# Kernel optimization log

Hardware: AMD Instinct MI355X
Metric: run time of the kernel (lower is better)

## Reference

```python
import jax, jax.numpy as jnp
import numpy as np

B, S, HID = 2, 2048, 3584
NH, NKV, HD = 16, 8, 256
WINDOW = 1024
SOFTCAP = 50.0


def setup_inputs() -> dict:
    key = jax.random.key(0)
    ks = jax.random.split(key, 8)
    hidden_states = jax.random.normal(ks[0], (B, S, HID), dtype=jnp.float32)
    attention_mask = jnp.ones((B, S), dtype=bool)
    position_ids = jnp.tile(jnp.arange(S, dtype=jnp.int32), (B, 1))
    # rotary tables indexed by position, last dim = head_dim
    inv_freq = 1.0 / (10000.0 ** (jnp.arange(0, HD, 2, dtype=jnp.float32) / HD))
    t = jnp.arange(S, dtype=jnp.float32)
    freqs = jnp.outer(t, inv_freq)  # [S, HD/2]
    emb = jnp.concatenate([freqs, freqs], axis=-1)  # [S, HD]
    sin, cos = jnp.sin(emb), jnp.cos(emb)
    causal_mask = jnp.tril(jnp.ones((1, 1, S, S), dtype=bool))
    sc = 0.02
    Wq = jax.random.normal(ks[1], (HID, NH * HD), dtype=jnp.float32) * sc
    Wk = jax.random.normal(ks[2], (HID, NKV * HD), dtype=jnp.float32) * sc
    Wv = jax.random.normal(ks[3], (HID, NKV * HD), dtype=jnp.float32) * sc
    Wo = jax.random.normal(ks[4], (NH * HD, HID), dtype=jnp.float32) * sc
    return {"hidden_states": hidden_states, "attention_mask": attention_mask,
            "position_ids": position_ids, "sin": sin, "cos": cos,
            "causal_mask": causal_mask, "Wq": Wq, "Wk": Wk, "Wv": Wv, "Wo": Wo}


def _rotate_half(x):
    x1, x2 = x[..., : x.shape[-1] // 2], x[..., x.shape[-1] // 2 :]
    return jnp.concatenate((-x2, x1), axis=-1)


def reference(hidden_states, attention_mask, position_ids, sin, cos, causal_mask, Wq, Wk, Wv, Wo):
    b, s, _ = hidden_states.shape
    q = (hidden_states @ Wq).reshape(b, s, NH, HD)
    k = (hidden_states @ Wk).reshape(b, s, NKV, HD)
    v = (hidden_states @ Wv).reshape(b, s, NKV, HD)

    # RoPE, applied in [b, h, s, d] layout as in the original
    s_ = sin[position_ids][:, None, :, :]  # [b,1,s,d]
    c_ = cos[position_ids][:, None, :, :]
    qh = q.transpose(0, 2, 1, 3)
    kh = k.transpose(0, 2, 1, 3)
    qh = qh * c_ + _rotate_half(qh) * s_
    kh = kh * c_ + _rotate_half(kh) * s_
    q = qh.transpose(0, 2, 1, 3)  # [b,s,nh,d]
    k = kh.transpose(0, 2, 1, 3)  # [b,s,nkv,d]

    # GQA: repeat kv heads to match query heads
    groups = NH // NKV
    k = jnp.repeat(k, groups, axis=2)  # [b,s,nh,d]
    v = jnp.repeat(v, groups, axis=2)

    # combine causal + padding masks, then sliding-window (even layer)
    mask = causal_mask[:, :, :s, :s] & attention_mask[:, None, None, :]  # [b,1,s,s]
    mask = jnp.broadcast_to(mask, (b, 1, s, s))
    far_past = jnp.tril(jnp.ones((s, s), dtype=bool), k=-WINDOW)[None, None]
    mask = mask & ~far_past

    neg = jnp.finfo(jnp.float32).min
    bias = jnp.where(mask, 0.0, neg).astype(jnp.float32)

    scale = HD ** -0.5
    logits = jnp.einsum("bqhd,bkhd->bhqk", q, k) * scale
    # Gemma2 logit softcapping
    logits = SOFTCAP * jnp.tanh(logits / SOFTCAP)
    logits = logits + bias
    probs = jax.nn.softmax(logits, axis=-1)
    out = jnp.einsum("bhqk,bkhd->bqhd", probs, v)
    out = out.reshape(b, s, NH * HD)
    return out @ Wo
```

## Files before the change

kernel.cpp:

```cpp
#include <hip/hip_runtime.h>
#include <hip/hip_bf16.h>

typedef __bf16 bf16x8_t __attribute__((ext_vector_type(8)));
typedef __bf16 bf16x4_t __attribute__((ext_vector_type(4)));
typedef short s16x4_t  __attribute__((ext_vector_type(4)));
typedef float f32x4_t  __attribute__((ext_vector_type(4)));

#define NB 2
#define NS 2048
#define NHID 3584
#define NHEADS 16
#define NKVH 8
#define DH 256
#define WIN 1024

__device__ __forceinline__ float bf2f(ushort u) {
  union { unsigned v; float f; } x; x.v = ((unsigned)u) << 16; return x.f;
}
__device__ __forceinline__ ushort f2bf(float f) {
  unsigned x = __builtin_bit_cast(unsigned, f);
  unsigned r = (x + 0x7fffu + ((x >> 16) & 1u)) >> 16;
  return (ushort)r;
}

__device__ __forceinline__ void gload16(const void* g, void* l) {
  __builtin_amdgcn_global_load_lds((const __attribute__((address_space(1))) void*)g,
                                   (__attribute__((address_space(3))) void*)l, 16, 0, 0);
}

__device__ __forceinline__ f32x4_t mfma_pv(s16x4_t a, s16x4_t b, f32x4_t c) {
#if __has_builtin(__builtin_amdgcn_mfma_f32_16x16x16_bf16)
  return __builtin_amdgcn_mfma_f32_16x16x16_bf16(
      __builtin_bit_cast(bf16x4_t, a), __builtin_bit_cast(bf16x4_t, b), c, 0, 0, 0);
#else
  return __builtin_amdgcn_mfma_f32_16x16x16bf16_1k(a, b, c, 0, 0, 0);
#endif
}

__device__ __forceinline__ float pexp(float s) {
  float e = __expf(fminf(s * 0.0025f, 80.f));
  float th = __fdividef(e - 1.f, e + 1.f);
  return __expf(50.f * th);
}

__global__ __launch_bounds__(256) void f32_to_bf16_kernel(const float* __restrict__ in,
                                                          ushort* __restrict__ out, int n4) {
  int i = (int)blockIdx.x * 256 + (int)threadIdx.x;
  if (i < n4) {
    float4 v = ((const float4*)in)[i];
    ushort4 o;
    o.x = f2bf(v.x); o.y = f2bf(v.y); o.z = f2bf(v.z); o.w = f2bf(v.w);
    ((ushort4*)out)[i] = o;
  }
}

__global__ __launch_bounds__(256) void transpose_f32_bf16(const float* __restrict__ in,
                                                          ushort* __restrict__ out,
                                                          int R, int Cc) {
  __shared__ ushort tile[64][72];
  const int t = threadIdx.x;
  const int ct = Cc >> 6;
  const int by = blockIdx.x / ct;
  const int bx = blockIdx.x % ct;
  const int r0 = by << 6, c0 = bx << 6;
#pragma unroll
  for (int i = 0; i < 16; ++i) {
    int idx = i * 256 + t;
    int r = idx >> 6, c = idx & 63;
    tile[r][c] = f2bf(in[(size_t)(r0 + r) * Cc + c0 + c]);
  }
  __syncthreads();
#pragma unroll
  for (int i = 0; i < 16; ++i) {
    int idx = i * 256 + t;
    int rr = idx >> 6, cc = idx & 63;
    out[(size_t)(c0 + rr) * R + r0 + cc] = tile[cc][rr];
  }
}

#define GSYNC1 do { __builtin_amdgcn_s_barrier(); \
    asm volatile("s_waitcnt lgkmcnt(0)" ::: "memory"); \
    __builtin_amdgcn_sched_barrier(0); } while (0)
#define GSYNC2(st) do { \
    if (st) asm volatile("s_waitcnt vmcnt(2)" ::: "memory"); \
    else    asm volatile("s_waitcnt vmcnt(0)" ::: "memory"); \
    __builtin_amdgcn_sched_barrier(0); \
    __builtin_amdgcn_s_barrier(); } while (0)

template <int EPI>
__global__ __launch_bounds__(512, 2) void gemm256(const ushort* __restrict__ A,
                                                  const ushort* __restrict__ Bt,
                                                  void* __restrict__ Cout,
                                                  const float* __restrict__ sinT,
                                                  const float* __restrict__ cosT,
                                                  int M, int N, int K) {
  __shared__ alignas(16) char lds[131072];
  const int t = threadIdx.x;
  const int lane = t & 63;
  const int wid = t >> 6;
  const int wm = wid >> 2;
  const int wn = wid & 3;
  const int g = lane >> 4;
  const int lr = lane & 15;
  const int lrow8 = lane >> 3;
  const int lp = (lane & 7) ^ lrow8;

  const int nbn = N >> 8;
  const int nwg = (int)gridDim.x;
  const int bid = (int)blockIdx.x;
  const int swz = (bid & 7) * (nwg >> 3) + (bid >> 3);
  const int bm = swz / nbn, bn = swz % nbn;
  const int m0 = bm << 8, n0 = bn << 8;

  f32x4_t acc[8][4] = {};
  const int T = K >> 6;

  auto stageA = [&](int q, int koff, int bufn) {
    int row = (q << 6) + (wid << 3) + lrow8;
    gload16(A + (size_t)(m0 + row) * K + koff + (lp << 3),
            lds + bufn * 32768 + (q << 13) + (wid << 10));
  };
  auto stageB = [&](int q, int koff, int bufn) {
    int row = (q << 6) + (wid << 3) + lrow8;
    gload16(Bt + (size_t)(n0 + row) * K + koff + (lp << 3),
            lds + 65536 + bufn * 32768 + (q << 13) + (wid << 10));
  };

#pragma unroll
  for (int q = 0; q < 4; ++q) { stageA(q, 0, 0); stageB(q, 0, 0); }
  asm volatile("s_waitcnt vmcnt(0)" ::: "memory");
  __builtin_amdgcn_s_barrier();

  for (int tt = 0; tt < T; ++tt) {
    const int bc = tt & 1;
    const int bnx = bc ^ 1;
    const bool st = (tt + 1 < T);
    const int kn = (tt + 1) << 6;
    const char* cA = lds + bc * 32768;
    const char* cB = lds + 65536 + bc * 32768;
    bf16x8_t af[4], bfv[4];

    auto ldA = [&](int i, int mh, int ks) {
      int row = (wm << 7) + (mh << 6) + (i << 4) + lr;
      af[i] = *(const bf16x8_t*)(cA + (row << 7) + (((ks << 6) + (g << 4)) ^ ((row & 7) << 4)));
    };
    auto ldB = [&](int j, int ks) {
      int row = (wn << 6) + (j << 4) + lr;
      bfv[j] = *(const bf16x8_t*)(cB + (row << 7) + (((ks << 6) + (g << 4)) ^ ((row & 7) << 4)));
    };

#pragma unroll
    for (int i = 0; i < 4; ++i) ldA(i, 0, 0);
#pragma unroll
    for (int j = 0; j < 4; ++j) ldB(j, 0);
    if (st) { stageA(0, kn, bnx); stageA(2, kn, bnx); }
    GSYNC1;
    __builtin_amdgcn_s_setprio(1);
#pragma unroll
    for (int i = 0; i < 4; ++i)
#pragma unroll
      for (int j = 0; j < 4; ++j)
        acc[i][j] = __builtin_amdgcn_mfma_f32_16x16x32_bf16(af[i], bfv[j], acc[i][j], 0, 0, 0);
    __builtin_amdgcn_s_setprio(0);
    GSYNC2(st);

#pragma unroll
    for (int i = 0; i < 4; ++i) ldA(i, 1, 0);
    if (st) { stageB(0, kn, bnx); stageB(1, kn, bnx); }
    GSYNC1;
    __builtin_amdgcn_s_setprio(1);
#pragma unroll
    for (int i = 0; i < 4; ++i)
#pragma unroll
      for (int j = 0; j < 4; ++j)
        acc[4 + i][j] = __builtin_amdgcn_mfma_f32_16x16x32_bf16(af[i], bfv[j], acc[4 + i][j], 0, 0, 0);
    __builtin_amdgcn_s_setprio(0);
    GSYNC2(st);

#pragma unroll
    for (int i = 0; i < 4; ++i) ldA(i, 0, 1);
#pragma unroll
    for (int j = 0; j < 4; ++j) ldB(j, 1);
    if (st) { stageB(2, kn, bnx); stageB(3, kn, bnx); }
    GSYNC1;
    __builtin_amdgcn_s_setprio(1);
#pragma unroll
    for (int i = 0; i < 4; ++i)
#pragma unroll
      for (int j = 0; j < 4; ++j)
        acc[i][j] = __builtin_amdgcn_mfma_f32_16x16x32_bf16(af[i], bfv[j], acc[i][j], 0, 0, 0);
    __builtin_amdgcn_s_setprio(0);
    GSYNC2(st);

#pragma unroll
    for (int i = 0; i < 4; ++i) ldA(i, 1, 1);
    if (st) { stageA(1, kn, bnx); stageA(3, kn, bnx); }
    GSYNC1;
    __builtin_amdgcn_s_setprio(1);
#pragma unroll
    for (int i = 0; i < 4; ++i)
#pragma unroll
      for (int j = 0; j < 4; ++j)
        acc[4 + i][j] = __builtin_amdgcn_mfma_f32_16x16x32_bf16(af[i], bfv[j], acc[4 + i][j], 0, 0, 0);
    __builtin_amdgcn_s_setprio(0);
    GSYNC2(st);
  }

  __syncthreads();
  const bool trstage = (EPI == 5) && (n0 >= 2048);
  if (trstage) {
#pragma unroll
    for (int i = 0; i < 8; ++i)
#pragma unroll
      for (int j = 0; j < 4; ++j) {
        int col = (wn << 6) + (j << 4) + lr;
#pragma unroll
        for (int r = 0; r < 4; ++r) {
          int row = (wm << 7) + (i << 4) + (g << 2) + r;
          *(ushort*)(lds + (col << 9) + ((row << 1) ^ ((col & 7) << 4))) = f2bf(acc[i][j][r]);
        }
      }
  } else {
#pragma unroll
    for (int i = 0; i < 8; ++i)
#pragma unroll
      for (int j = 0; j < 4; ++j) {
        int col = (wn << 6) + (j << 4) + lr;
#pragma unroll
        for (int r = 0; r < 4; ++r) {
          int row = (wm << 7) + (i << 4) + (g << 2) + r;
          *(ushort*)(lds + (row << 9) + ((col << 1) ^ ((row & 7) << 4))) = f2bf(acc[i][j][r]);
        }
      }
  }
  __syncthreads();

  auto ropeStore = [&](ushort* C, int ldc) {
#pragma unroll
    for (int it = 0; it < 16; ++it) {
      int idx = it * 512 + t;
      int row = idx >> 5, ch = idx & 31;
      uint4 v = *(const uint4*)(lds + (row << 9) + ((ch << 4) ^ ((row & 7) << 4)));
      uint4 p = *(const uint4*)(lds + (row << 9) + (((ch ^ 16) << 4) ^ ((row & 7) << 4)));
      int pos = (m0 + row) & (NS - 1);
      int d0 = ch << 3;
      float4 c0 = *(const float4*)(cosT + (size_t)pos * 256 + d0);
      float4 c1 = *(const float4*)(cosT + (size_t)pos * 256 + d0 + 4);
      float4 s0 = *(const float4*)(sinT + (size_t)pos * 256 + d0);
      float4 s1 = *(const float4*)(sinT + (size_t)pos * 256 + d0 + 4);
      float cs[8] = {c0.x, c0.y, c0.z, c0.w, c1.x, c1.y, c1.z, c1.w};
      float ss[8] = {s0.x, s0.y, s0.z, s0.w, s1.x, s1.y, s1.z, s1.w};
      const float sgn = (ch < 16) ? -1.f : 1.f;
      const ushort* vv = (const ushort*)&v;
      const ushort* pp = (const ushort*)&p;
      ushort o[8];
#pragma unroll
      for (int e = 0; e < 8; ++e)
        o[e] = f2bf(bf2f(vv[e]) * cs[e] + sgn * bf2f(pp[e]) * ss[e]);
      *(uint4*)(C + (size_t)(m0 + row) * ldc + n0 % ((EPI == 5) ? 2048 : (1 << 30)) + (ch << 3)) = *(const uint4*)o;
    }
  };

  if (EPI == 1) {
    ushort* C = (ushort*)Cout;
#pragma unroll
    for (int it = 0; it < 16; ++it) {
      int idx = it * 512 + t;
      int row = idx >> 5, ch = idx & 31;
      uint4 v = *(const uint4*)(lds + (row << 9) + ((ch << 4) ^ ((row & 7) << 4)));
      uint4 p = *(const uint4*)(lds + (row << 9) + (((ch ^ 16) << 4) ^ ((row & 7) << 4)));
      int pos = (m0 + row) & (NS - 1);
      int d0 = ch << 3;
      float4 c0 = *(const float4*)(cosT + (size_t)pos * 256 + d0);
      float4 c1 = *(const float4*)(cosT + (size_t)pos * 256 + d0 + 4);
      float4 s0 = *(const float4*)(sinT + (size_t)pos * 256 + d0);
      float4 s1 = *(const float4*)(sinT + (size_t)pos * 256 + d0 + 4);
      float cs[8] = {c0.x, c0.y, c0.z, c0.w, c1.x, c1.y, c1.z, c1.w};
      float ss[8] = {s0.x, s0.y, s0.z, s0.w, s1.x, s1.y, s1.z, s1.w};
      const float sgn = (ch < 16) ? -1.f : 1.f;
      const ushort* vv = (const ushort*)&v;
      const ushort* pp = (const ushort*)&p;
      ushort o[8];
#pragma unroll
      for (int e = 0; e < 8; ++e)
        o[e] = f2bf(bf2f(vv[e]) * cs[e] + sgn * bf2f(pp[e]) * ss[e]);
      *(uint4*)(C + (size_t)(m0 + row) * N + n0 + (ch << 3)) = *(const uint4*)o;
    }
  } else if (EPI == 5) {
    ushort* C = (ushort*)Cout;
    if (n0 < 2048) {
#pragma unroll
      for (int it = 0; it < 16; ++it) {
        int idx = it * 512 + t;
        int row = idx >> 5, ch = idx & 31;
        uint4 v = *(const uint4*)(lds + (row << 9) + ((ch << 4) ^ ((row & 7) << 4)));
        uint4 p = *(const uint4*)(lds + (row << 9) + (((ch ^ 16) << 4) ^ ((row & 7) << 4)));
        int pos = (m0 + row) & (NS - 1);
        int d0 = ch << 3;
        float4 c0 = *(const float4*)(cosT + (size_t)pos * 256 + d0);
        float4 c1 = *(const float4*)(cosT + (size_t)pos * 256 + d0 + 4);
        float4 s0 = *(const float4*)(sinT + (size_t)pos * 256 + d0);
        float4 s1 = *(const float4*)(sinT + (size_t)pos * 256 + d0 + 4);
        float cs[8] = {c0.x, c0.y, c0.z, c0.w, c1.x, c1.y, c1.z, c1.w};
        float ss[8] = {s0.x, s0.y, s0.z, s0.w, s1.x, s1.y, s1.z, s1.w};
        const float sgn = (ch < 16) ? -1.f : 1.f;
        const ushort* vv = (const ushort*)&v;
        const ushort* pp = (const ushort*)&p;
        ushort o[8];
#pragma unroll
        for (int e = 0; e < 8; ++e)
          o[e] = f2bf(bf2f(vv[e]) * cs[e] + sgn * bf2f(pp[e]) * ss[e]);
        *(uint4*)(C + (size_t)(m0 + row) * 2048 + n0 + (ch << 3)) = *(const uint4*)o;
      }
    } else {
      ushort* vC = C + (size_t)4096 * 2048;
      const int plane = (m0 >> 11) * NKVH + ((n0 - 2048) >> 8);
      ushort* dst = vC + (size_t)plane * ((size_t)NS * DH) + (size_t)((m0 & (NS - 1)) >> 5) * 8192;
#pragma unroll
      for (int it = 0; it < 16; ++it) {
        int s = it * 512 + t;
        int lr2 = s & 7, kq = (s >> 3) & 7, dt_l = (s >> 6) & 15, sb_l = s >> 10;
        int d0 = (dt_l << 4) + (lr2 << 1);
        int r0 = (sb_l << 5) + (kq << 2);
        uint2 a = *(const uint2*)(lds + (d0 << 9) + ((r0 << 1) ^ ((d0 & 7) << 4)));
        uint2 b2 = *(const uint2*)(lds + ((d0 + 1) << 9) + ((r0 << 1) ^ (((d0 + 1) & 7) << 4)));
        uint4 v; v.x = a.x; v.y = a.y; v.z = b2.x; v.w = b2.y;
        *(uint4*)(dst + (size_t)s * 8) = v;
      }
    }
  } else {
    float* Cf = (float*)Cout;
#pragma unroll
    for (int it = 0; it < 32; ++it) {
      int idx = it * 512 + t;
      int row = idx >> 6, qd = idx & 63;
      ushort4 hv = *(const ushort4*)(lds + (row << 9) + ((qd << 3) ^ ((row & 7) << 4)));
      float4 fv;
      fv.x = bf2f(hv.x); fv.y = bf2f(hv.y); fv.z = bf2f(hv.z); fv.w = bf2f(hv.w);
      *(float4*)(Cf + (size_t)(m0 + row) * N + n0 + (qd << 2)) = fv;
    }
  }
}

__global__ __launch_bounds__(512) void attn_kernel(const ushort* __restrict__ q,
                                                   const ushort* __restrict__ k,
                                                   const ushort* __restrict__ vt,
                                                   ushort* __restrict__ ao) {
  __shared__ alignas(16) char lK[2][16384];
  __shared__ alignas(16) char lV[2][16384];
  const int bid = (int)blockIdx.x;
  const int qb = bid & 15;
  const int h = (bid >> 4) & 15;
  const int b = bid >> 8;
  const int kvh = h >> 1;
  const int qb0 = qb << 7;
  const int t = threadIdx.x;
  const int lane = t & 63;
  const int w = t >> 6;
  const int g = lane >> 4;
  const int lr = lane & 15;

  const int qrow = qb0 + (w << 4) + lr;
  bf16x8_t qf[8];
  const ushort* qbase = q + (size_t)(b * NS + qrow) * (NHEADS * DH) + h * DH;
#pragma unroll
  for (int ks = 0; ks < 8; ++ks)
    qf[ks] = *(const bf16x8_t*)(qbase + (ks << 5) + (g << 3));

  float l_r = 0.f;
  f32x4_t oacc[16] = {};

  const int qminw = qb0 + (w << 4);
  const int qmaxw = qminw + 15;
  int t_lo = qb0 - (WIN - 1);
  if (t_lo < 0) t_lo = 0;
  t_lo &= ~31;
  const int t_hi = qb0 + 127;
  const int nt = ((t_hi - t_lo) >> 5) + 1;

  const ushort* kgb = k + (size_t)(b * NS) * (NKVH * DH) + kvh * DH;
  const ushort* vgb = vt + (size_t)(b * NKVH + kvh) * ((size_t)NS * DH);

  auto stage = [&](int kt, int bi) {
    char* dk = lK[bi];
    char* dv = lV[bi];
    const int sb = kt >> 5;
#pragma unroll
    for (int j = 0; j < 2; ++j) {
      int i = (w << 1) + j;
      int row = (i << 1) + (lane >> 5);
      int ck = (lane & 31) ^ (row & 7);
      gload16(kgb + (size_t)(kt + row) * (NKVH * DH) + (ck << 3), dk + (i << 10));
      gload16(vgb + (size_t)sb * 8192 + (((i << 6) + lane) << 3), dv + (i << 10));
    }
  };

  int cur = 0;
  stage(t_lo, 0);
  __syncthreads();

  for (int i = 0; i < nt; ++i) {
    const int kt = t_lo + (i << 5);
    if (i + 1 < nt) stage(kt + 32, cur ^ 1);
    const char* lk = lK[cur];
    const char* lv = lV[cur];
#pragma unroll
    for (int sub = 0; sub < 2; ++sub) {
      const int key0 = kt + (sub << 4);
      if (key0 > qmaxw) continue;
      if (key0 + 15 < qminw - (WIN - 1)) continue;

      f32x4_t sacc = {};
      __builtin_amdgcn_s_setprio(1);
#pragma unroll
      for (int ks = 0; ks < 8; ++ks) {
        int row = (sub << 4) + lr;
        bf16x8_t kf = *(const bf16x8_t*)(lk + (((row << 9) + (ks << 6) + (g << 4)) ^ ((row & 7) << 4)));
        sacc = __builtin_amdgcn_mfma_f32_16x16x32_bf16(kf, qf[ks], sacc, 0, 0, 0);
      }
      __builtin_amdgcn_s_setprio(0);

      float pvv[4];
      const bool full = (key0 + 15 <= qminw) && (key0 >= qmaxw - (WIN - 1));
      if (full) {
#pragma unroll
        for (int r = 0; r < 4; ++r) { pvv[r] = pexp(sacc[r]); l_r += pvv[r]; }
      } else {
#pragma unroll
        for (int r = 0; r < 4; ++r) {
          int key = key0 + (g << 2) + r;
          bool ok = (key <= qrow) && (qrow - key < WIN);
          pvv[r] = ok ? pexp(sacc[r]) : 0.f;
          l_r += pvv[r];
        }
      }

      s16x4_t pa;
      pa[0] = (short)f2bf(pvv[0]);
      pa[1] = (short)f2bf(pvv[1]);
      pa[2] = (short)f2bf(pvv[2]);
      pa[3] = (short)f2bf(pvv[3]);

      const int kqoff = ((sub << 2) + g) << 7;
      __builtin_amdgcn_s_setprio(1);
#pragma unroll
      for (int dt = 0; dt < 16; ++dt) {
        s16x4_t vf = *(const s16x4_t*)(lv + (dt << 10) + kqoff + (lr << 3));
        oacc[dt] = mfma_pv(pa, vf, oacc[dt]);
      }
      __builtin_amdgcn_s_setprio(0);
    }
    __syncthreads();
    cur ^= 1;
  }

  l_r += __shfl_xor(l_r, 16);
  l_r += __shfl_xor(l_r, 32);
  float dn[4];
#pragma unroll
  for (int r = 0; r < 4; ++r)
    dn[r] = 1.0f / __shfl(l_r, (g << 2) + r);

  const int orow0 = b * NS + qb0 + (w << 4) + (g << 2);
#pragma unroll
  for (int dt = 0; dt < 16; ++dt) {
    int col = h * DH + (dt << 4) + lr;
#pragma unroll
    for (int r = 0; r < 4; ++r) {
      ao[(size_t)(orow0 + r) * (NHEADS * DH) + col] = f2bf(oacc[dt][r] * dn[r]);
    }
  }
}

extern "C" void kernel_launch(void* const* d_in, const int* in_sizes, int n_in,
                              void* d_out, int out_size, void* d_ws, size_t ws_size,
                              hipStream_t stream) {
  const float* hs   = (const float*)d_in[0];
  const float* sint = (const float*)d_in[3];
  const float* cost = (const float*)d_in[4];
  const float* Wq = (const float*)d_in[6];
  const float* Wk = (const float*)d_in[7];
  const float* Wv = (const float*)d_in[8];
  const float* Wo = (const float*)d_in[9];

  char* ws = (char*)d_ws;
  size_t off = 0;
  auto alloc = [&](size_t bytes) {
    char* p = ws + off;
    off += (bytes + 255) & ~(size_t)255;
    return p;
  };
  ushort* hsb   = (ushort*)alloc((size_t)4096 * 3584 * 2);
  ushort* wT    = (ushort*)alloc((size_t)4096 * 3584 * 2);
  ushort* qbuf  = (ushort*)alloc((size_t)4096 * 4096 * 2);
  ushort* kbuf  = (ushort*)alloc((size_t)4096 * 2048 * 2);
  ushort* vtbuf = (ushort*)alloc((size_t)4096 * 2048 * 2);
  ushort* aobuf = qbuf;
  if (off > ws_size) return;

  f32_to_bf16_kernel<<<(4096 * 3584 / 4) / 256, 256, 0, stream>>>(hs, hsb, 4096 * 3584 / 4);

  transpose_f32_bf16<<<(3584 / 64) * (2048 / 64), 256, 0, stream>>>(Wk, wT, 3584, 2048);
  transpose_f32_bf16<<<(3584 / 64) * (2048 / 64), 256, 0, stream>>>(Wv, wT + (size_t)2048 * 3584, 3584, 2048);
  gemm256<5><<<16 * 16, 512, 0, stream>>>(hsb, wT, kbuf, sint, cost, 4096, 4096, 3584);

  transpose_f32_bf16<<<(3584 / 64) * (4096 / 64), 256, 0, stream>>>(Wq, wT, 3584, 4096);
  gemm256<1><<<16 * 16, 512, 0, stream>>>(hsb, wT, qbuf, sint, cost, 4096, 4096, 3584);

  attn_kernel<<<NB * NHEADS * (NS / 128), 512, 0, stream>>>(qbuf, kbuf, vtbuf, aobuf);

  transpose_f32_bf16<<<(4096 / 64) * (3584 / 64), 256, 0, stream>>>(Wo, wT, 4096, 3584);
  gemm256<2><<<16 * 14, 512, 0, stream>>>(aobuf, wT, d_out, nullptr, nullptr, 4096, 3584, 4096);
}
```

Baseline: 587.3 us.

## Halve attention query tile to 64 rows and reorder blocks for load balance

The attention kernel now uses 64-row query tiles with 256 threads per block, doubling the grid to 1024 blocks. Block IDs are remapped so expensive late-sequence tiles are scheduled first, paired head blocks share a KV plane, and cheaper early tiles fill in later, aiming to balance the sliding-window workload across CUs and improve L2 reuse of K/V. Each block stages K/V with more loads per thread. Smaller tiles mean K/V is reloaded from memory more often per query row. An unused ropeStore lambda is also removed.

```diff
diff --git a/kernel.cpp b/kernel.cpp
--- a/kernel.cpp
+++ b/kernel.cpp
@@ -235,7 +235,8 @@
   }
   __syncthreads();
 
-  auto ropeStore = [&](ushort* C, int ldc) {
+  if (EPI == 1) {
+    ushort* C = (ushort*)Cout;
 #pragma unroll
     for (int it = 0; it < 16; ++it) {
       int idx = it * 512 + t;
@@ -257,33 +258,6 @@
 #pragma unroll
       for (int e = 0; e < 8; ++e)
         o[e] = f2bf(bf2f(vv[e]) * cs[e] + sgn * bf2f(pp[e]) * ss[e]);
-      *(uint4*)(C + (size_t)(m0 + row) * ldc + n0 % ((EPI == 5) ? 2048 : (1 << 30)) + (ch << 3)) = *(const uint4*)o;
-    }
-  };
-
-  if (EPI == 1) {
-    ushort* C = (ushort*)Cout;
-#pragma unroll
-    for (int it = 0; it < 16; ++it) {
-      int idx = it * 512 + t;
-      int row = idx >> 5, ch = idx & 31;
-      uint4 v = *(const uint4*)(lds + (row << 9) + ((ch << 4) ^ ((row & 7) << 4)));
-      uint4 p = *(const uint4*)(lds + (row << 9) + (((ch ^ 16) << 4) ^ ((row & 7) << 4)));
-      int pos = (m0 + row) & (NS - 1);
-      int d0 = ch << 3;
-      float4 c0 = *(const float4*)(cosT + (size_t)pos * 256 + d0);
-      float4 c1 = *(const float4*)(cosT + (size_t)pos * 256 + d0 + 4);
-      float4 s0 = *(const float4*)(sinT + (size_t)pos * 256 + d0);
-      float4 s1 = *(const float4*)(sinT + (size_t)pos * 256 + d0 + 4);
-      float cs[8] = {c0.x, c0.y, c0.z, c0.w, c1.x, c1.y, c1.z, c1.w};
-      float ss[8] = {s0.x, s0.y, s0.z, s0.w, s1.x, s1.y, s1.z, s1.w};
-      const float sgn = (ch < 16) ? -1.f : 1.f;
-      const ushort* vv = (const ushort*)&v;
-      const ushort* pp = (const ushort*)&p;
-      ushort o[8];
-#pragma unroll
-      for (int e = 0; e < 8; ++e)
-        o[e] = f2bf(bf2f(vv[e]) * cs[e] + sgn * bf2f(pp[e]) * ss[e]);
       *(uint4*)(C + (size_t)(m0 + row) * N + n0 + (ch << 3)) = *(const uint4*)o;
     }
   } else if (EPI == 5) {
@@ -342,18 +316,28 @@
   }
 }
 
-__global__ __launch_bounds__(512) void attn_kernel(const ushort* __restrict__ q,
+__global__ __launch_bounds__(256) void attn_kernel(const ushort* __restrict__ q,
                                                    const ushort* __restrict__ k,
                                                    const ushort* __restrict__ vt,
                                                    ushort* __restrict__ ao) {
   __shared__ alignas(16) char lK[2][16384];
   __shared__ alignas(16) char lV[2][16384];
   const int bid = (int)blockIdx.x;
-  const int qb = bid & 15;
-  const int h = (bid >> 4) & 15;
-  const int b = bid >> 8;
-  const int kvh = h >> 1;
-  const int qb0 = qb << 7;
+  const int x = bid & 7;
+  const int s_ = bid >> 3;
+  const int rnd = s_ >> 5;
+  const int c = s_ & 31;
+  const int a = c >> 1;
+  const int hl = c & 1;
+  const int plane = (x << 1) | (rnd & 1);
+  int qb;
+  if (rnd < 2) qb = 16 + a;
+  else if (rnd == 2) qb = a;
+  else qb = 15 - a;
+  const int b = plane >> 3;
+  const int kvh = plane & 7;
+  const int h = (kvh << 1) | hl;
+  const int qb0 = qb << 6;
   const int t = threadIdx.x;
   const int lane = t & 63;
   const int w = t >> 6;
@@ -375,7 +359,7 @@
   int t_lo = qb0 - (WIN - 1);
   if (t_lo < 0) t_lo = 0;
   t_lo &= ~31;
-  const int t_hi = qb0 + 127;
+  const int t_hi = qb0 + 63;
   const int nt = ((t_hi - t_lo) >> 5) + 1;
 
   const ushort* kgb = k + (size_t)(b * NS) * (NKVH * DH) + kvh * DH;
@@ -386,8 +370,8 @@
     char* dv = lV[bi];
     const int sb = kt >> 5;
 #pragma unroll
-    for (int j = 0; j < 2; ++j) {
-      int i = (w << 1) + j;
+    for (int j = 0; j < 4; ++j) {
+      int i = (w << 2) + j;
       int row = (i << 1) + (lane >> 5);
       int ck = (lane & 31) ^ (row & 7);
       gload16(kgb + (size_t)(kt + row) * (NKVH * DH) + (ck << 3), dk + (i << 10));
@@ -507,7 +491,7 @@
   transpose_f32_bf16<<<(3584 / 64) * (4096 / 64), 256, 0, stream>>>(Wq, wT, 3584, 4096);
   gemm256<1><<<16 * 16, 512, 0, stream>>>(hsb, wT, qbuf, sint, cost, 4096, 4096, 3584);
 
-  attn_kernel<<<NB * NHEADS * (NS / 128), 512, 0, stream>>>(qbuf, kbuf, vtbuf, aobuf);
+  attn_kernel<<<NB * NHEADS * (NS / 64), 256, 0, stream>>>(qbuf, kbuf, vtbuf, aobuf);
 
   transpose_f32_bf16<<<(4096 / 64) * (3584 / 64), 256, 0, stream>>>(Wo, wT, 4096, 3584);
   gemm256<2><<<16 * 14, 512, 0, stream>>>(aobuf, wT, d_out, nullptr, nullptr, 4096, 3584, 4096);
```

Result: faster. 564.3 us (-3.9%).
